# Kernel optimization log

Measured on AMD Instinct MI355X. Metric: run time of the kernel, lower is better.

Reference implementation:

```python
import jax, jax.numpy as jnp
import numpy as np

NUM_HEADS = 16
HEAD_DIM = 64
MAX_REL = 128
NEG_INF = -1e30


def setup_inputs() -> dict:
    key = jax.random.key(0)
    ks = jax.random.split(key, 5)
    B, L, D = 2, 2048, 1024
    x = jax.random.normal(ks[0], (B, L, D), dtype=jnp.float32)
    key_padding_mask = jnp.zeros((B, L), dtype=bool)  # True = padded
    Wqkv = jax.random.normal(ks[1], (D, 3 * D), dtype=jnp.float32) * (D ** -0.5)
    bqkv = jnp.zeros((3 * D,), dtype=jnp.float32)
    Wout = jax.random.normal(ks[2], (D, D), dtype=jnp.float32) * (D ** -0.5)
    bout = jnp.zeros((D,), dtype=jnp.float32)
    bias_table = jax.random.normal(ks[3], (2 * MAX_REL + 1, NUM_HEADS), dtype=jnp.float32) * 0.02
    return {"x": x, "key_padding_mask": key_padding_mask, "Wqkv": Wqkv,
            "bqkv": bqkv, "Wout": Wout, "bout": bout, "bias_table": bias_table}


def _rel_bias(bias_table, L):
    # relative position index: clamp(k - q, -MAX_REL, MAX_REL) + MAX_REL -> [L, L]
    rel = jnp.arange(L)[None, :] - jnp.arange(L)[:, None]
    idx = jnp.clip(rel, -MAX_REL, MAX_REL) + MAX_REL
    return bias_table[idx].transpose(2, 0, 1)  # [H, L, L]


def reference(x, key_padding_mask, Wqkv, bqkv, Wout, bout, bias_table):
    B, L, D = x.shape
    H, hd = NUM_HEADS, HEAD_DIM
    qkv = x @ Wqkv + bqkv                      # [B, L, 3D]
    q, k, v = jnp.split(qkv, 3, axis=-1)
    q = q.reshape(B, L, H, hd).transpose(0, 2, 1, 3)  # [B, H, L, hd]
    k = k.reshape(B, L, H, hd).transpose(0, 2, 1, 3)
    v = v.reshape(B, L, H, hd).transpose(0, 2, 1, 3)
    scores = jnp.einsum('bhqd,bhkd->bhqk', q, k) * (hd ** -0.5)
    scores = scores + _rel_bias(bias_table, L)[None]   # [B, H, L, L]
    scores = jnp.where(key_padding_mask[:, None, None, :], NEG_INF, scores)
    attn = jax.nn.softmax(scores, axis=-1)
    out = jnp.einsum('bhqk,bhkd->bhqd', attn, v)       # [B, H, L, hd]
    out = out.transpose(0, 2, 1, 3).reshape(B, L, D)
    return out @ Wout + bout
```

## Files before the change

### kernel.cpp

```cpp
#include <hip/hip_runtime.h>
#include <hip/hip_bf16.h>
#include <stdint.h>

#define LSEQ 2048
#define BATCH 2
#define DMODEL 1024
#define NH 16
#define HD 64

typedef __attribute__((ext_vector_type(8))) short bf16x8;
typedef __attribute__((ext_vector_type(4))) float f32x4;

__device__ __forceinline__ short f2bf(float f) {
  union { float f; uint32_t u; } v; v.f = f;
  uint32_t r = v.u + 0x8000u;
  return (short)(r >> 16);
}

__device__ __forceinline__ uint32_t pack_bf16(float lo, float hi) {
  union { float f; uint32_t u; } a, b; a.f = lo; b.f = hi;
  uint32_t al = (a.u + 0x8000u) >> 16;
  uint32_t bh = (b.u + 0x8000u) & 0xFFFF0000u;
  return al | bh;
}

__device__ __forceinline__ float exp2_fast(float x) {
#if __has_builtin(__builtin_amdgcn_exp2f)
  return __builtin_amdgcn_exp2f(x);
#else
  float r; asm("v_exp_f32 %0, %1" : "=v"(r) : "v"(x)); return r;
#endif
}

__device__ __forceinline__ void gll16(const void* g, void* l) {
  __builtin_amdgcn_global_load_lds(
      (const __attribute__((address_space(1))) void*)g,
      (__attribute__((address_space(3))) void*)l, 16, 0, 0);
}

__global__ void prep_kernel(const float* __restrict__ x, const float* __restrict__ Wqkv,
                            const float* __restrict__ Wout, short* __restrict__ xbf,
                            short* __restrict__ wqkvT, short* __restrict__ woutT) {
  __shared__ float tile[32][33];
  const int bid = blockIdx.x;
  if (bid < 4096) {
    int i = (bid * 256 + threadIdx.x) * 4;
    float4 v = *(const float4*)(x + i);
    short4 o;
    o.x = f2bf(v.x); o.y = f2bf(v.y); o.z = f2bf(v.z); o.w = f2bf(v.w);
    *(short4*)(xbf + i) = o;
    return;
  }
  const float* in; short* out; int K, N, t;
  if (bid < 7168) { in = Wqkv; out = wqkvT; K = 1024; N = 3072; t = bid - 4096; }
  else            { in = Wout; out = woutT; K = 1024; N = 1024; t = bid - 7168; }
  int kb = (t & 31) * 32, nb = (t >> 5) * 32;
  int tx = threadIdx.x & 31, ty = threadIdx.x >> 5;
  #pragma unroll
  for (int i = ty; i < 32; i += 8)
    tile[i][tx] = in[(size_t)(kb + i) * N + nb + tx];
  __syncthreads();
  #pragma unroll
  for (int i = ty; i < 32; i += 8)
    out[(size_t)(nb + i) * K + kb + tx] = f2bf(tile[tx][i]);
}

template <int EPI>
__global__ __launch_bounds__(256, 2) void gemm_bt(
    const short* __restrict__ A, const short* __restrict__ Bt,
    const float* __restrict__ bias, float* __restrict__ outf,
    short* __restrict__ q_out, short* __restrict__ k_out, short* __restrict__ v_out) {
  constexpr int K = 1024, BK = 64, NKT = K / BK;
  __shared__ short Als[2][128 * BK];
  __shared__ short Bls[2][128 * BK];
  const int tid = threadIdx.x;
  const int lane = tid & 63;
  const int c = lane & 15, g = lane >> 4;
  const int m0 = blockIdx.x * 128;
  const int n0 = blockIdx.y * 128;
  const int wid = tid >> 6;
  const int wm = (wid >> 1) * 64, wn = (wid & 1) * 64;

  f32x4 acc[4][4] = {};

  auto stage = [&](int kt, int bbuf) {
    const int k0 = kt * BK;
    #pragma unroll
    for (int inst = 0; inst < 4; ++inst) {
      int i = inst * 256 + tid;
      int row = i >> 3, cg = i & 7;
      int scc = cg ^ (row & 7);
      gll16(A + (size_t)(m0 + row) * K + k0 + scc * 8, &Als[bbuf][i * 8]);
      gll16(Bt + (size_t)(n0 + row) * K + k0 + scc * 8, &Bls[bbuf][i * 8]);
    }
  };

  stage(0, 0);

  for (int kt = 0; kt < NKT; ++kt) {
    const int bb = kt & 1;
    asm volatile("s_waitcnt vmcnt(0)" ::: "memory");
    __builtin_amdgcn_s_barrier();
    if (kt < NKT - 1) stage(kt + 1, bb ^ 1);

    #pragma unroll
    for (int ks = 0; ks < 2; ++ks) {
      const int kb = ks * 64 + g * 16;
      bf16x8 af[4], bfv[4];
      #pragma unroll
      for (int m = 0; m < 4; ++m) {
        int row = wm + m * 16 + c;
        af[m] = *(const bf16x8*)((const char*)&Als[bb][0] + row * 128 + (kb ^ ((row & 7) << 4)));
      }
      #pragma unroll
      for (int n = 0; n < 4; ++n) {
        int row = wn + n * 16 + c;
        bfv[n] = *(const bf16x8*)((const char*)&Bls[bb][0] + row * 128 + (kb ^ ((row & 7) << 4)));
      }
      __builtin_amdgcn_s_setprio(1);
      #pragma unroll
      for (int m = 0; m < 4; ++m)
        #pragma unroll
        for (int n = 0; n < 4; ++n)
          acc[m][n] = __builtin_amdgcn_mfma_f32_16x16x32_bf16(af[m], bfv[n], acc[m][n], 0, 0, 0);
      __builtin_amdgcn_s_setprio(0);
    }
  }

  #pragma unroll
  for (int m = 0; m < 4; ++m) {
    #pragma unroll
    for (int n = 0; n < 4; ++n) {
      #pragma unroll
      for (int r = 0; r < 4; ++r) {
        int row = m0 + wm + m * 16 + g * 4 + r;
        int col = n0 + wn + n * 16 + c;
        float val = acc[m][n][r] + bias[col];
        if (EPI == 1) {
          outf[(size_t)row * DMODEL + col] = val;
        } else {
          int b = row >> 11, l = row & 2047;
          int which = col >> 10, rem = col & 1023;
          int hn = rem >> 6, d = rem & 63;
          size_t bh = (size_t)b * NH + hn;
          if (which == 0)       q_out[(bh * LSEQ + l) * HD + d] = f2bf(val * 0.1803368801f);
          else if (which == 1)  k_out[(bh * LSEQ + l) * HD + d] = f2bf(val);
          else                  v_out[(bh * HD + d) * LSEQ + l] = f2bf(val);
        }
      }
    }
  }
}

__global__ __launch_bounds__(256, 2) void attn_kernel(
    const short* __restrict__ qb, const short* __restrict__ kb,
    const short* __restrict__ vtb, const unsigned char* __restrict__ kpm,
    const float* __restrict__ bias_table, short* __restrict__ ob) {
  constexpr int NT = LSEQ / 64;
  __shared__ short Kls[2][64 * 64];
  __shared__ short Vls[2][64 * 64];
  __shared__ uint2 Pls[4][512];
  __shared__ float biasc[257];
  __shared__ unsigned mbits_s;

  const int tid = threadIdx.x, lane = tid & 63, wid = tid >> 6;
  const int g = lane >> 4, c = lane & 15;
  const int lin = blockIdx.x;
  const int swz = (lin & 7) * 64 + (lin >> 3);
  const int q0 = (swz & 15) * 128;
  const int h = (swz >> 4) & 15;
  const int b = swz >> 8;
  const size_t bh = (size_t)b * NH + h;
  const short* qbase = qb + bh * LSEQ * HD;
  const short* kbase = kb + bh * LSEQ * HD;
  const short* vbase = vtb + bh * HD * LSEQ;
  const unsigned char* kpmb = kpm + (size_t)b * LSEQ;

  bf16x8 qf[2][2];
  #pragma unroll
  for (int qg = 0; qg < 2; ++qg)
    #pragma unroll
    for (int ks = 0; ks < 2; ++ks) {
      int qrow = q0 + wid * 32 + qg * 16 + c;
      qf[qg][ks] = *(const bf16x8*)(qbase + (size_t)qrow * HD + ks * 32 + g * 8);
    }

  if (tid < 32) {
    const uint4* mp = (const uint4*)(kpmb + tid * 64);
    uint4 m0 = mp[0], m1 = mp[1], m2 = mp[2], m3 = mp[3];
    unsigned anyb = m0.x | m0.y | m0.z | m0.w | m1.x | m1.y | m1.z | m1.w |
                    m2.x | m2.y | m2.z | m2.w | m3.x | m3.y | m3.z | m3.w;
    unsigned long long bal = __ballot(anyb != 0);
    if (tid == 0) mbits_s = (unsigned)bal;
  }
  for (int i = tid; i < 257; i += 256) biasc[i] = bias_table[i * NH + h] * 1.44269504f;
  __syncthreads();
  const unsigned mbits = mbits_s;
  const float cb_lo = biasc[0], cb_hi = biasc[256];

  auto stage = [&](int t, int bbuf) {
    const int kv0s = t * 64;
    #pragma unroll
    for (int inst = 0; inst < 2; ++inst) {
      int cc0 = inst * 256 + tid;
      int row = cc0 >> 3, cc = cc0 & 7;
      int scc = cc ^ (row & 7);
      gll16(kbase + (size_t)(kv0s + row) * HD + scc * 8, &Kls[bbuf][cc0 * 8]);
      gll16(vbase + (size_t)row * LSEQ + kv0s + scc * 8, &Vls[bbuf][cc0 * 8]);
    }
  };

  f32x4 o[4][2], l_acc[2];
  #pragma unroll
  for (int nt = 0; nt < 4; ++nt)
    #pragma unroll
    for (int qg = 0; qg < 2; ++qg) o[nt][qg] = (f32x4){0.f, 0.f, 0.f, 0.f};
  l_acc[0] = (f32x4){0.f, 0.f, 0.f, 0.f};
  l_acc[1] = (f32x4){0.f, 0.f, 0.f, 0.f};

  bf16x8 onesf;
  #pragma unroll
  for (int j = 0; j < 8; ++j) onesf[j] = (short)0x3F80;

  uint2* pw = &Pls[wid][0];
  const int c7s = (c & 7) << 4;
  const int cx  = (c & 7) << 1;

  stage(0, 0);

  for (int t = 0; t < NT; ++t) {
    const int bb = t & 1;
    const int kv0 = t * 64;
    asm volatile("s_waitcnt vmcnt(0)" ::: "memory");
    __builtin_amdgcn_s_barrier();
    if (t < NT - 1) stage(t + 1, bb ^ 1);

    f32x4 st[4][2];
    __builtin_amdgcn_s_setprio(1);
    #pragma unroll
    for (int nt = 0; nt < 4; ++nt) {
      f32x4 a0 = {}, a1 = {};
      #pragma unroll
      for (int ks = 0; ks < 2; ++ks) {
        int krow = nt * 16 + c;
        int kbyte = ks * 64 + g * 16;
        const bf16x8 kf =
            *(const bf16x8*)((const char*)&Kls[bb][0] + krow * 128 + (kbyte ^ c7s));
        a0 = __builtin_amdgcn_mfma_f32_16x16x32_bf16(kf, qf[0][ks], a0, 0, 0, 0);
        a1 = __builtin_amdgcn_mfma_f32_16x16x32_bf16(kf, qf[1][ks], a1, 0, 0, 0);
      }
      st[nt][0] = a0; st[nt][1] = a1;
    }
    __builtin_amdgcn_s_setprio(0);

    const int dw = kv0 - q0 - wid * 32;
    if (dw >= 160 || dw <= -192) {
      const float cb = dw > 0 ? cb_hi : cb_lo;
      #pragma unroll
      for (int nt = 0; nt < 4; ++nt)
        #pragma unroll
        for (int qg = 0; qg < 2; ++qg)
          #pragma unroll
          for (int r = 0; r < 4; ++r) st[nt][qg][r] += cb;
    } else {
      #pragma unroll
      for (int nt = 0; nt < 4; ++nt)
        #pragma unroll
        for (int qg = 0; qg < 2; ++qg) {
          const int base = dw + nt * 16 + g * 4 - qg * 16 - c;
          #pragma unroll
          for (int r = 0; r < 4; ++r) {
            int rel = base + r;
            rel = rel < -128 ? -128 : (rel > 128 ? 128 : rel);
            st[nt][qg][r] += biasc[rel + 128];
          }
        }
    }
    if (mbits & (1u << t)) {
      #pragma unroll
      for (int nt = 0; nt < 4; ++nt)
        #pragma unroll
        for (int r = 0; r < 4; ++r) {
          float mk = kpmb[kv0 + nt * 16 + g * 4 + r] ? -1e30f : 0.f;
          st[nt][0][r] += mk;
          st[nt][1][r] += mk;
        }
    }

    #pragma unroll
    for (int qg = 0; qg < 2; ++qg)
      #pragma unroll
      for (int nt = 0; nt < 4; ++nt) {
        uint2 w;
        w.x = pack_bf16(exp2_fast(st[nt][qg][0]), exp2_fast(st[nt][qg][1]));
        w.y = pack_bf16(exp2_fast(st[nt][qg][2]), exp2_fast(st[nt][qg][3]));
        pw[(qg * 16 + c) * 16 + ((nt * 4 + g) ^ cx)] = w;
      }

    #pragma unroll
    for (int ks = 0; ks < 2; ++ks) {
      const int pu = (ks * 8 + g * 2) ^ cx;
      union { uint2 u[2]; bf16x8 v; } pa0u, pa1u;
      pa0u.u[0] = pw[c * 16 + pu];        pa0u.u[1] = pw[c * 16 + pu + 1];
      pa1u.u[0] = pw[(16 + c) * 16 + pu]; pa1u.u[1] = pw[(16 + c) * 16 + pu + 1];
      const bf16x8 pa0 = pa0u.v, pa1 = pa1u.v;
      l_acc[0] = __builtin_amdgcn_mfma_f32_16x16x32_bf16(pa0, onesf, l_acc[0], 0, 0, 0);
      l_acc[1] = __builtin_amdgcn_mfma_f32_16x16x32_bf16(pa1, onesf, l_acc[1], 0, 0, 0);
      const int pbyte = ks * 64 + g * 16;
      #pragma unroll
      for (int nt = 0; nt < 4; ++nt) {
        int vrow = nt * 16 + c;
        const bf16x8 vf =
            *(const bf16x8*)((const char*)&Vls[bb][0] + vrow * 128 + (pbyte ^ c7s));
        o[nt][0] = __builtin_amdgcn_mfma_f32_16x16x32_bf16(pa0, vf, o[nt][0], 0, 0, 0);
        o[nt][1] = __builtin_amdgcn_mfma_f32_16x16x32_bf16(pa1, vf, o[nt][1], 0, 0, 0);
      }
    }
  }

  #pragma unroll
  for (int qg = 0; qg < 2; ++qg)
    #pragma unroll
    for (int r = 0; r < 4; ++r) {
      float inv = 1.f / l_acc[qg][r];
      int qrow = q0 + wid * 32 + qg * 16 + g * 4 + r;
      size_t obase = ((size_t)b * LSEQ + qrow) * DMODEL + (size_t)h * HD;
      #pragma unroll
      for (int nt = 0; nt < 4; ++nt)
        ob[obase + nt * 16 + c] = f2bf(o[nt][qg][r] * inv);
    }
}

extern "C" void kernel_launch(void* const* d_in, const int* in_sizes, int n_in,
                              void* d_out, int out_size, void* d_ws, size_t ws_size,
                              hipStream_t stream) {
  (void)in_sizes; (void)n_in; (void)out_size; (void)ws_size;
  const float* x = (const float*)d_in[0];
  const unsigned char* kpm = (const unsigned char*)d_in[1];
  const float* Wqkv = (const float*)d_in[2];
  const float* bqkv = (const float*)d_in[3];
  const float* Wout = (const float*)d_in[4];
  const float* bout = (const float*)d_in[5];
  const float* btab = (const float*)d_in[6];
  float* out = (float*)d_out;

  short* ws = (short*)d_ws;
  short* xbf   = ws;
  short* wqkvT = xbf + 4194304;
  short* woutT = wqkvT + 3145728;
  short* qbuf  = woutT + 1048576;
  short* kbuf  = qbuf + 4194304;
  short* vtbuf = kbuf + 4194304;
  short* obuf  = vtbuf + 4194304;

  prep_kernel<<<dim3(8192), dim3(256), 0, stream>>>(x, Wqkv, Wout, xbf, wqkvT, woutT);

  gemm_bt<0><<<dim3(32, 24), dim3(256), 0, stream>>>(xbf, wqkvT, bqkv, nullptr,
                                                     qbuf, kbuf, vtbuf);
  attn_kernel<<<dim3(512), dim3(256), 0, stream>>>(qbuf, kbuf, vtbuf, kpm, btab, obuf);
  gemm_bt<1><<<dim3(32, 8), dim3(256), 0, stream>>>(obuf, woutT, bout, out,
                                                    nullptr, nullptr, nullptr);
}
```

Baseline: 131.6 us.

## Switch attention to 32x32x16 MFMA and pass P through lane shuffles instead of LDS

The attention inner loop now uses 32x32x16 bf16 MFMA tiles instead of 16x16x32. Because the score accumulator layout of the larger tile nearly matches the A-operand layout needed for P·V, the P fragment is rebuilt with cross-half-wave shuffles rather than a write and read round trip through shared memory. This drops the per-wave P buffer and its LDS traffic and issues fewer, larger MFMAs. In exchange it adds shuffle and select work, and the output store pattern changes.

After: 136.1 us. +3.5%, slower.

```diff
diff --git a/kernel.cpp b/kernel.cpp
--- a/kernel.cpp
+++ b/kernel.cpp
@@ -10,6 +10,7 @@
 
 typedef __attribute__((ext_vector_type(8))) short bf16x8;
 typedef __attribute__((ext_vector_type(4))) float f32x4;
+typedef __attribute__((ext_vector_type(16))) float f32x16;
 
 __device__ __forceinline__ short f2bf(float f) {
   union { float f; uint32_t u; } v; v.f = f;
@@ -159,12 +160,12 @@
   constexpr int NT = LSEQ / 64;
   __shared__ short Kls[2][64 * 64];
   __shared__ short Vls[2][64 * 64];
-  __shared__ uint2 Pls[4][512];
   __shared__ float biasc[257];
   __shared__ unsigned mbits_s;
 
   const int tid = threadIdx.x, lane = tid & 63, wid = tid >> 6;
-  const int g = lane >> 4, c = lane & 15;
+  const int l31 = lane & 31, hi = lane >> 5;
+  const bool hib = hi != 0;
   const int lin = blockIdx.x;
   const int swz = (lin & 7) * 64 + (lin >> 3);
   const int q0 = (swz & 15) * 128;
@@ -176,14 +177,11 @@
   const short* vbase = vtb + bh * HD * LSEQ;
   const unsigned char* kpmb = kpm + (size_t)b * LSEQ;
 
-  bf16x8 qf[2][2];
-  #pragma unroll
-  for (int qg = 0; qg < 2; ++qg)
-    #pragma unroll
-    for (int ks = 0; ks < 2; ++ks) {
-      int qrow = q0 + wid * 32 + qg * 16 + c;
-      qf[qg][ks] = *(const bf16x8*)(qbase + (size_t)qrow * HD + ks * 32 + g * 8);
-    }
+  const int qrow_frag = q0 + wid * 32 + l31;
+  bf16x8 qf[4];
+  #pragma unroll
+  for (int ds = 0; ds < 4; ++ds)
+    qf[ds] = *(const bf16x8*)(qbase + (size_t)qrow_frag * HD + ds * 16 + hi * 8);
 
   if (tid < 32) {
     const uint4* mp = (const uint4*)(kpmb + tid * 64);
@@ -210,21 +208,12 @@
     }
   };
 
-  f32x4 o[4][2], l_acc[2];
-  #pragma unroll
-  for (int nt = 0; nt < 4; ++nt)
-    #pragma unroll
-    for (int qg = 0; qg < 2; ++qg) o[nt][qg] = (f32x4){0.f, 0.f, 0.f, 0.f};
-  l_acc[0] = (f32x4){0.f, 0.f, 0.f, 0.f};
-  l_acc[1] = (f32x4){0.f, 0.f, 0.f, 0.f};
+  f32x16 o32[2] = {};
+  f32x16 l32 = {};
 
   bf16x8 onesf;
   #pragma unroll
   for (int j = 0; j < 8; ++j) onesf[j] = (short)0x3F80;
-
-  uint2* pw = &Pls[wid][0];
-  const int c7s = (c & 7) << 4;
-  const int cx  = (c & 7) << 1;
 
   stage(0, 0);
 
@@ -235,100 +224,81 @@
     __builtin_amdgcn_s_barrier();
     if (t < NT - 1) stage(t + 1, bb ^ 1);
 
-    f32x4 st[4][2];
-    __builtin_amdgcn_s_setprio(1);
-    #pragma unroll
-    for (int nt = 0; nt < 4; ++nt) {
-      f32x4 a0 = {}, a1 = {};
-      #pragma unroll
-      for (int ks = 0; ks < 2; ++ks) {
-        int krow = nt * 16 + c;
-        int kbyte = ks * 64 + g * 16;
-        const bf16x8 kf =
-            *(const bf16x8*)((const char*)&Kls[bb][0] + krow * 128 + (kbyte ^ c7s));
-        a0 = __builtin_amdgcn_mfma_f32_16x16x32_bf16(kf, qf[0][ks], a0, 0, 0, 0);
-        a1 = __builtin_amdgcn_mfma_f32_16x16x32_bf16(kf, qf[1][ks], a1, 0, 0, 0);
-      }
-      st[nt][0] = a0; st[nt][1] = a1;
-    }
-    __builtin_amdgcn_s_setprio(0);
-
-    const int dw = kv0 - q0 - wid * 32;
-    if (dw >= 160 || dw <= -192) {
-      const float cb = dw > 0 ? cb_hi : cb_lo;
-      #pragma unroll
-      for (int nt = 0; nt < 4; ++nt)
-        #pragma unroll
-        for (int qg = 0; qg < 2; ++qg)
-          #pragma unroll
-          for (int r = 0; r < 4; ++r) st[nt][qg][r] += cb;
-    } else {
-      #pragma unroll
-      for (int nt = 0; nt < 4; ++nt)
-        #pragma unroll
-        for (int qg = 0; qg < 2; ++qg) {
-          const int base = dw + nt * 16 + g * 4 - qg * 16 - c;
-          #pragma unroll
-          for (int r = 0; r < 4; ++r) {
-            int rel = base + r;
-            rel = rel < -128 ? -128 : (rel > 128 ? 128 : rel);
-            st[nt][qg][r] += biasc[rel + 128];
-          }
+    #pragma unroll
+    for (int kh = 0; kh < 2; ++kh) {
+      f32x16 stv = {};
+      __builtin_amdgcn_s_setprio(1);
+      #pragma unroll
+      for (int ds = 0; ds < 4; ++ds) {
+        const int krow = 32 * kh + l31;
+        const bf16x8 kf = *(const bf16x8*)((const char*)&Kls[bb][0] + krow * 128 +
+                                           ((ds * 32 + hi * 16) ^ ((krow & 7) << 4)));
+        stv = __builtin_amdgcn_mfma_f32_32x32x16_bf16(kf, qf[ds], stv, 0, 0, 0);
+      }
+      __builtin_amdgcn_s_setprio(0);
+
+      const int dq = kv0 + 32 * kh - q0 - wid * 32;
+      float p[16];
+      if (dq >= 159 || dq <= -159) {
+        const float cb = dq > 0 ? cb_hi : cb_lo;
+        #pragma unroll
+        for (int rg = 0; rg < 16; ++rg) p[rg] = stv[rg] + cb;
+      } else {
+        const int base = dq + 4 * hi - l31;
+        #pragma unroll
+        for (int rg = 0; rg < 16; ++rg) {
+          int rel = base + (rg & 3) + 8 * (rg >> 2);
+          rel = rel < -128 ? -128 : (rel > 128 ? 128 : rel);
+          p[rg] = stv[rg] + biasc[rel + 128];
         }
-    }
-    if (mbits & (1u << t)) {
-      #pragma unroll
-      for (int nt = 0; nt < 4; ++nt)
-        #pragma unroll
-        for (int r = 0; r < 4; ++r) {
-          float mk = kpmb[kv0 + nt * 16 + g * 4 + r] ? -1e30f : 0.f;
-          st[nt][0][r] += mk;
-          st[nt][1][r] += mk;
+      }
+      if (mbits & (1u << t)) {
+        #pragma unroll
+        for (int rg = 0; rg < 16; ++rg)
+          p[rg] += kpmb[kv0 + 32 * kh + (rg & 3) + 8 * (rg >> 2) + 4 * hi] ? -1e30f : 0.f;
+      }
+
+      uint32_t W[4][2];
+      #pragma unroll
+      for (int s = 0; s < 4; ++s)
+        #pragma unroll
+        for (int u = 0; u < 2; ++u)
+          W[s][u] = pack_bf16(exp2_fast(p[4 * s + 2 * u]), exp2_fast(p[4 * s + 2 * u + 1]));
+
+      #pragma unroll
+      for (int ktp = 0; ktp < 2; ++ktp) {
+        const int kt = 2 * kh + ktp;
+        const int se = 2 * ktp, so = 2 * ktp + 1;
+        uint32_t recv0 = __shfl_xor(hib ? W[se][0] : W[so][0], 32);
+        uint32_t recv1 = __shfl_xor(hib ? W[se][1] : W[so][1], 32);
+        union { uint32_t u[4]; bf16x8 v; } pa;
+        pa.u[0] = hib ? recv0    : W[se][0];
+        pa.u[1] = hib ? recv1    : W[se][1];
+        pa.u[2] = hib ? W[so][0] : recv0;
+        pa.u[3] = hib ? W[so][1] : recv1;
+
+        __builtin_amdgcn_s_setprio(1);
+        l32 = __builtin_amdgcn_mfma_f32_32x32x16_bf16(pa.v, onesf, l32, 0, 0, 0);
+        #pragma unroll
+        for (int dt = 0; dt < 2; ++dt) {
+          const int vrow = l31 + 32 * dt;
+          const bf16x8 vf = *(const bf16x8*)((const char*)&Vls[bb][0] + vrow * 128 +
+                                             ((kt * 32 + hi * 16) ^ ((vrow & 7) << 4)));
+          o32[dt] = __builtin_amdgcn_mfma_f32_32x32x16_bf16(pa.v, vf, o32[dt], 0, 0, 0);
         }
-    }
-
-    #pragma unroll
-    for (int qg = 0; qg < 2; ++qg)
-      #pragma unroll
-      for (int nt = 0; nt < 4; ++nt) {
-        uint2 w;
-        w.x = pack_bf16(exp2_fast(st[nt][qg][0]), exp2_fast(st[nt][qg][1]));
-        w.y = pack_bf16(exp2_fast(st[nt][qg][2]), exp2_fast(st[nt][qg][3]));
-        pw[(qg * 16 + c) * 16 + ((nt * 4 + g) ^ cx)] = w;
-      }
-
-    #pragma unroll
-    for (int ks = 0; ks < 2; ++ks) {
-      const int pu = (ks * 8 + g * 2) ^ cx;
-      union { uint2 u[2]; bf16x8 v; } pa0u, pa1u;
-      pa0u.u[0] = pw[c * 16 + pu];        pa0u.u[1] = pw[c * 16 + pu + 1];
-      pa1u.u[0] = pw[(16 + c) * 16 + pu]; pa1u.u[1] = pw[(16 + c) * 16 + pu + 1];
-      const bf16x8 pa0 = pa0u.v, pa1 = pa1u.v;
-      l_acc[0] = __builtin_amdgcn_mfma_f32_16x16x32_bf16(pa0, onesf, l_acc[0], 0, 0, 0);
-      l_acc[1] = __builtin_amdgcn_mfma_f32_16x16x32_bf16(pa1, onesf, l_acc[1], 0, 0, 0);
-      const int pbyte = ks * 64 + g * 16;
-      #pragma unroll
-      for (int nt = 0; nt < 4; ++nt) {
-        int vrow = nt * 16 + c;
-        const bf16x8 vf =
-            *(const bf16x8*)((const char*)&Vls[bb][0] + vrow * 128 + (pbyte ^ c7s));
-        o[nt][0] = __builtin_amdgcn_mfma_f32_16x16x32_bf16(pa0, vf, o[nt][0], 0, 0, 0);
-        o[nt][1] = __builtin_amdgcn_mfma_f32_16x16x32_bf16(pa1, vf, o[nt][1], 0, 0, 0);
-      }
-    }
-  }
-
-  #pragma unroll
-  for (int qg = 0; qg < 2; ++qg)
-    #pragma unroll
-    for (int r = 0; r < 4; ++r) {
-      float inv = 1.f / l_acc[qg][r];
-      int qrow = q0 + wid * 32 + qg * 16 + g * 4 + r;
-      size_t obase = ((size_t)b * LSEQ + qrow) * DMODEL + (size_t)h * HD;
-      #pragma unroll
-      for (int nt = 0; nt < 4; ++nt)
-        ob[obase + nt * 16 + c] = f2bf(o[nt][qg][r] * inv);
-    }
+        __builtin_amdgcn_s_setprio(0);
+      }
+    }
+  }
+
+  #pragma unroll
+  for (int rg = 0; rg < 16; ++rg) {
+    const int qrow = q0 + wid * 32 + (rg & 3) + 8 * (rg >> 2) + 4 * hi;
+    const float inv = 1.f / l32[rg];
+    const size_t obase = ((size_t)b * LSEQ + qrow) * DMODEL + (size_t)h * HD + l31;
+    ob[obase]      = f2bf(o32[0][rg] * inv);
+    ob[obase + 32] = f2bf(o32[1][rg] * inv);
+  }
 }
 
 extern "C" void kernel_launch(void* const* d_in, const int* in_sizes, int n_in,
```

## Split attention KV range in two with partial outputs and merge kernel

Applied to the files above, without the earlier changes.

Adds an attention variant that splits each query block's key/value range into two halves. This doubles the block count to 1024, and the kernel runs at a launch bound of 4 blocks per CU with single-buffered K/V LDS. Each half writes unnormalized fp32 partial outputs and row sums, and a separate merge kernel adds them, normalizes, and writes bf16. The aim is more parallelism and occupancy, paid for with extra fp32 global traffic, a second launch, and the loss of the K/V prefetch double buffering. The path is used only when the workspace is large enough; otherwise the original kernel runs.

Result: slower. 149.1 us (+13.4%).

```diff
diff --git a/kernel.cpp b/kernel.cpp
--- a/kernel.cpp
+++ b/kernel.cpp
@@ -152,7 +152,8 @@
   }
 }
 
-__global__ __launch_bounds__(256, 2) void attn_kernel(
+
+__global__ __launch_bounds__(256, 2) void attn_mono(
     const short* __restrict__ qb, const short* __restrict__ kb,
     const short* __restrict__ vtb, const unsigned char* __restrict__ kpm,
     const float* __restrict__ bias_table, short* __restrict__ ob) {
@@ -331,10 +332,212 @@
     }
 }
 
+__global__ __launch_bounds__(256, 4) void attn_split(
+    const short* __restrict__ qb, const short* __restrict__ kb,
+    const short* __restrict__ vtb, const unsigned char* __restrict__ kpm,
+    const float* __restrict__ bias_table, float* __restrict__ part_o,
+    float* __restrict__ part_l) {
+  constexpr int NTL = 16;
+  __shared__ short Kls[64 * 64];
+  __shared__ short Vls[64 * 64];
+  __shared__ uint2 Pls[4][512];
+  __shared__ float biasc[257];
+  __shared__ unsigned mbits_s;
+
+  const int tid = threadIdx.x, lane = tid & 63, wid = tid >> 6;
+  const int g = lane >> 4, c = lane & 15;
+  const int lin = blockIdx.x;
+  const int swz = (lin & 7) * 128 + (lin >> 3);
+  const int q0 = (swz & 15) * 128;
+  const int h = (swz >> 4) & 15;
+  const int b = (swz >> 8) & 1;
+  const int split = swz >> 9;
+  const int kvbase = split * (LSEQ / 2);
+  const size_t bh = (size_t)b * NH + h;
+  const short* qbase = qb + bh * LSEQ * HD;
+  const short* kbase = kb + bh * LSEQ * HD;
+  const short* vbase = vtb + bh * HD * LSEQ;
+  const unsigned char* kpmb = kpm + (size_t)b * LSEQ;
+
+  bf16x8 qf[2][2];
+  #pragma unroll
+  for (int qg = 0; qg < 2; ++qg)
+    #pragma unroll
+    for (int ks = 0; ks < 2; ++ks) {
+      int qrow = q0 + wid * 32 + qg * 16 + c;
+      qf[qg][ks] = *(const bf16x8*)(qbase + (size_t)qrow * HD + ks * 32 + g * 8);
+    }
+
+  if (tid < 32) {
+    const uint4* mp = (const uint4*)(kpmb + tid * 64);
+    uint4 m0 = mp[0], m1 = mp[1], m2 = mp[2], m3 = mp[3];
+    unsigned anyb = m0.x | m0.y | m0.z | m0.w | m1.x | m1.y | m1.z | m1.w |
+                    m2.x | m2.y | m2.z | m2.w | m3.x | m3.y | m3.z | m3.w;
+    unsigned long long bal = __ballot(anyb != 0);
+    if (tid == 0) mbits_s = (unsigned)bal;
+  }
+  for (int i = tid; i < 257; i += 256) biasc[i] = bias_table[i * NH + h] * 1.44269504f;
+  __syncthreads();
+  const unsigned mbits = mbits_s;
+  const float cb_lo = biasc[0], cb_hi = biasc[256];
+
+  auto stage = [&](int t) {
+    const int kv0s = kvbase + t * 64;
+    #pragma unroll
+    for (int inst = 0; inst < 2; ++inst) {
+      int cc0 = inst * 256 + tid;
+      int row = cc0 >> 3, cc = cc0 & 7;
+      int scc = cc ^ (row & 7);
+      gll16(kbase + (size_t)(kv0s + row) * HD + scc * 8, &Kls[cc0 * 8]);
+      gll16(vbase + (size_t)row * LSEQ + kv0s + scc * 8, &Vls[cc0 * 8]);
+    }
+  };
+
+  f32x4 o[4][2], l_acc[2];
+  #pragma unroll
+  for (int nt = 0; nt < 4; ++nt)
+    #pragma unroll
+    for (int qg = 0; qg < 2; ++qg) o[nt][qg] = (f32x4){0.f, 0.f, 0.f, 0.f};
+  l_acc[0] = (f32x4){0.f, 0.f, 0.f, 0.f};
+  l_acc[1] = (f32x4){0.f, 0.f, 0.f, 0.f};
+
+  bf16x8 onesf;
+  #pragma unroll
+  for (int j = 0; j < 8; ++j) onesf[j] = (short)0x3F80;
+
+  uint2* pw = &Pls[wid][0];
+  const int c7s = (c & 7) << 4;
+  const int cx  = (c & 7) << 1;
+
+  for (int t = 0; t < NTL; ++t) {
+    const int kv0 = kvbase + t * 64;
+    __builtin_amdgcn_s_barrier();
+    stage(t);
+    asm volatile("s_waitcnt vmcnt(0)" ::: "memory");
+    __builtin_amdgcn_s_barrier();
+
+    f32x4 st[4][2];
+    __builtin_amdgcn_s_setprio(1);
+    #pragma unroll
+    for (int nt = 0; nt < 4; ++nt) {
+      f32x4 a0 = {}, a1 = {};
+      #pragma unroll
+      for (int ks = 0; ks < 2; ++ks) {
+        int krow = nt * 16 + c;
+        int kbyte = ks * 64 + g * 16;
+        const bf16x8 kf =
+            *(const bf16x8*)((const char*)&Kls[0] + krow * 128 + (kbyte ^ c7s));
+        a0 = __builtin_amdgcn_mfma_f32_16x16x32_bf16(kf, qf[0][ks], a0, 0, 0, 0);
+        a1 = __builtin_amdgcn_mfma_f32_16x16x32_bf16(kf, qf[1][ks], a1, 0, 0, 0);
+      }
+      st[nt][0] = a0; st[nt][1] = a1;
+    }
+    __builtin_amdgcn_s_setprio(0);
+
+    const int dw = kv0 - q0 - wid * 32;
+    if (dw >= 160 || dw <= -192) {
+      const float cb = dw > 0 ? cb_hi : cb_lo;
+      #pragma unroll
+      for (int nt = 0; nt < 4; ++nt)
+        #pragma unroll
+        for (int qg = 0; qg < 2; ++qg)
+          #pragma unroll
+          for (int r = 0; r < 4; ++r) st[nt][qg][r] += cb;
+    } else {
+      #pragma unroll
+      for (int nt = 0; nt < 4; ++nt)
+        #pragma unroll
+        for (int qg = 0; qg < 2; ++qg) {
+          const int base = dw + nt * 16 + g * 4 - qg * 16 - c;
+          #pragma unroll
+          for (int r = 0; r < 4; ++r) {
+            int rel = base + r;
+            rel = rel < -128 ? -128 : (rel > 128 ? 128 : rel);
+            st[nt][qg][r] += biasc[rel + 128];
+          }
+        }
+    }
+    if (mbits & (1u << (kv0 >> 6))) {
+      #pragma unroll
+      for (int nt = 0; nt < 4; ++nt)
+        #pragma unroll
+        for (int r = 0; r < 4; ++r) {
+          float mk = kpmb[kv0 + nt * 16 + g * 4 + r] ? -1e30f : 0.f;
+          st[nt][0][r] += mk;
+          st[nt][1][r] += mk;
+        }
+    }
+
+    #pragma unroll
+    for (int qg = 0; qg < 2; ++qg)
+      #pragma unroll
+      for (int nt = 0; nt < 4; ++nt) {
+        uint2 w;
+        w.x = pack_bf16(exp2_fast(st[nt][qg][0]), exp2_fast(st[nt][qg][1]));
+        w.y = pack_bf16(exp2_fast(st[nt][qg][2]), exp2_fast(st[nt][qg][3]));
+        pw[(qg * 16 + c) * 16 + ((nt * 4 + g) ^ cx)] = w;
+      }
+
+    #pragma unroll
+    for (int ks = 0; ks < 2; ++ks) {
+      const int pu = (ks * 8 + g * 2) ^ cx;
+      union { uint2 u[2]; bf16x8 v; } pa0u, pa1u;
+      pa0u.u[0] = pw[c * 16 + pu];        pa0u.u[1] = pw[c * 16 + pu + 1];
+      pa1u.u[0] = pw[(16 + c) * 16 + pu]; pa1u.u[1] = pw[(16 + c) * 16 + pu + 1];
+      const bf16x8 pa0 = pa0u.v, pa1 = pa1u.v;
+      l_acc[0] = __builtin_amdgcn_mfma_f32_16x16x32_bf16(pa0, onesf, l_acc[0], 0, 0, 0);
+      l_acc[1] = __builtin_amdgcn_mfma_f32_16x16x32_bf16(pa1, onesf, l_acc[1], 0, 0, 0);
+      const int pbyte = ks * 64 + g * 16;
+      #pragma unroll
+      for (int nt = 0; nt < 4; ++nt) {
+        int vrow = nt * 16 + c;
+        const bf16x8 vf =
+            *(const bf16x8*)((const char*)&Vls[0] + vrow * 128 + (pbyte ^ c7s));
+        o[nt][0] = __builtin_amdgcn_mfma_f32_16x16x32_bf16(pa0, vf, o[nt][0], 0, 0, 0);
+        o[nt][1] = __builtin_amdgcn_mfma_f32_16x16x32_bf16(pa1, vf, o[nt][1], 0, 0, 0);
+      }
+    }
+  }
+
+  float* po = part_o + (size_t)split * (BATCH * NH * LSEQ) * HD;
+  float* pl = part_l + (size_t)split * (BATCH * NH * LSEQ);
+  #pragma unroll
+  for (int qg = 0; qg < 2; ++qg)
+    #pragma unroll
+    for (int r = 0; r < 4; ++r) {
+      int qrow = q0 + wid * 32 + qg * 16 + g * 4 + r;
+      size_t row = bh * LSEQ + qrow;
+      #pragma unroll
+      for (int nt = 0; nt < 4; ++nt)
+        po[row * HD + nt * 16 + c] = o[nt][qg][r];
+      if (c == 0) pl[row] = l_acc[qg][r];
+    }
+}
+
+__global__ void merge_kernel(const float* __restrict__ part_o,
+                             const float* __restrict__ part_l,
+                             short* __restrict__ ob) {
+  constexpr size_t HALF = (size_t)BATCH * NH * LSEQ * HD;
+  constexpr size_t ROWS = (size_t)BATCH * NH * LSEQ;
+  size_t i = ((size_t)blockIdx.x * 256 + threadIdx.x) * 4;
+  size_t row = i >> 6;
+  float4 a = *(const float4*)(part_o + i);
+  float4 bvec = *(const float4*)(part_o + HALF + i);
+  float inv = 1.f / (part_l[row] + part_l[ROWS + row]);
+  int bi = (int)(row >> 15), h = (int)((row >> 11) & 15), q = (int)(row & 2047);
+  size_t oidx = (((size_t)bi * LSEQ + q) * DMODEL) + (size_t)h * HD + (i & 63);
+  short4 o;
+  o.x = f2bf((a.x + bvec.x) * inv);
+  o.y = f2bf((a.y + bvec.y) * inv);
+  o.z = f2bf((a.z + bvec.z) * inv);
+  o.w = f2bf((a.w + bvec.w) * inv);
+  *(short4*)(ob + oidx) = o;
+}
+
 extern "C" void kernel_launch(void* const* d_in, const int* in_sizes, int n_in,
                               void* d_out, int out_size, void* d_ws, size_t ws_size,
                               hipStream_t stream) {
-  (void)in_sizes; (void)n_in; (void)out_size; (void)ws_size;
+  (void)in_sizes; (void)n_in; (void)out_size;
   const float* x = (const float*)d_in[0];
   const unsigned char* kpm = (const unsigned char*)d_in[1];
   const float* Wqkv = (const float*)d_in[2];
@@ -352,12 +555,21 @@
   short* kbuf  = qbuf + 4194304;
   short* vtbuf = kbuf + 4194304;
   short* obuf  = vtbuf + 4194304;
+  float* part_o = (float*)(obuf + 4194304);
+  float* part_l = part_o + 2 * (size_t)4194304;
+  const size_t need = (size_t)(obuf + 4194304 - ws) * 2 + 8388608ull * 4 + 131072ull * 4 * 2;
 
   prep_kernel<<<dim3(8192), dim3(256), 0, stream>>>(x, Wqkv, Wout, xbf, wqkvT, woutT);
 
   gemm_bt<0><<<dim3(32, 24), dim3(256), 0, stream>>>(xbf, wqkvT, bqkv, nullptr,
                                                      qbuf, kbuf, vtbuf);
-  attn_kernel<<<dim3(512), dim3(256), 0, stream>>>(qbuf, kbuf, vtbuf, kpm, btab, obuf);
+  if (ws_size >= need) {
+    attn_split<<<dim3(1024), dim3(256), 0, stream>>>(qbuf, kbuf, vtbuf, kpm, btab,
+                                                     part_o, part_l);
+    merge_kernel<<<dim3(4096), dim3(256), 0, stream>>>(part_o, part_l, obuf);
+  } else {
+    attn_mono<<<dim3(512), dim3(256), 0, stream>>>(qbuf, kbuf, vtbuf, kpm, btab, obuf);
+  }
   gemm_bt<1><<<dim3(32, 8), dim3(256), 0, stream>>>(obuf, woutT, bout, out,
                                                     nullptr, nullptr, nullptr);
 }
```

## Load K/V fragments directly from global memory instead of LDS staging

Applied to the files above, without the earlier changes.

Removes the double-buffered LDS staging of K and V tiles, along with the per-tile barrier and wait. Each wave now reads its MFMA operand fragments straight from global memory into registers, and the PV MFMA block is raised to high priority. The aim is to drop LDS traffic and block-wide synchronisation. The cost is that each wave refetches K/V that was previously shared across 4 waves, and load latency is no longer hidden by prefetching.

Measured after the change: 192.4 us. +46.3%, slower.

```diff
diff --git a/kernel.cpp b/kernel.cpp
--- a/kernel.cpp
+++ b/kernel.cpp
@@ -157,8 +157,6 @@
     const short* __restrict__ vtb, const unsigned char* __restrict__ kpm,
     const float* __restrict__ bias_table, short* __restrict__ ob) {
   constexpr int NT = LSEQ / 64;
-  __shared__ short Kls[2][64 * 64];
-  __shared__ short Vls[2][64 * 64];
   __shared__ uint2 Pls[4][512];
   __shared__ float biasc[257];
   __shared__ unsigned mbits_s;
@@ -198,18 +196,6 @@
   const unsigned mbits = mbits_s;
   const float cb_lo = biasc[0], cb_hi = biasc[256];
 
-  auto stage = [&](int t, int bbuf) {
-    const int kv0s = t * 64;
-    #pragma unroll
-    for (int inst = 0; inst < 2; ++inst) {
-      int cc0 = inst * 256 + tid;
-      int row = cc0 >> 3, cc = cc0 & 7;
-      int scc = cc ^ (row & 7);
-      gll16(kbase + (size_t)(kv0s + row) * HD + scc * 8, &Kls[bbuf][cc0 * 8]);
-      gll16(vbase + (size_t)row * LSEQ + kv0s + scc * 8, &Vls[bbuf][cc0 * 8]);
-    }
-  };
-
   f32x4 o[4][2], l_acc[2];
   #pragma unroll
   for (int nt = 0; nt < 4; ++nt)
@@ -223,17 +209,18 @@
   for (int j = 0; j < 8; ++j) onesf[j] = (short)0x3F80;
 
   uint2* pw = &Pls[wid][0];
-  const int c7s = (c & 7) << 4;
-  const int cx  = (c & 7) << 1;
-
-  stage(0, 0);
+  const int cx = (c & 7) << 1;
 
   for (int t = 0; t < NT; ++t) {
-    const int bb = t & 1;
     const int kv0 = t * 64;
-    asm volatile("s_waitcnt vmcnt(0)" ::: "memory");
-    __builtin_amdgcn_s_barrier();
-    if (t < NT - 1) stage(t + 1, bb ^ 1);
+
+    bf16x8 kfr[4][2];
+    #pragma unroll
+    for (int nt = 0; nt < 4; ++nt)
+      #pragma unroll
+      for (int ks = 0; ks < 2; ++ks)
+        kfr[nt][ks] = *(const bf16x8*)(kbase + (size_t)(kv0 + nt * 16 + c) * HD +
+                                       ks * 32 + g * 8);
 
     f32x4 st[4][2];
     __builtin_amdgcn_s_setprio(1);
@@ -242,12 +229,8 @@
       f32x4 a0 = {}, a1 = {};
       #pragma unroll
       for (int ks = 0; ks < 2; ++ks) {
-        int krow = nt * 16 + c;
-        int kbyte = ks * 64 + g * 16;
-        const bf16x8 kf =
-            *(const bf16x8*)((const char*)&Kls[bb][0] + krow * 128 + (kbyte ^ c7s));
-        a0 = __builtin_amdgcn_mfma_f32_16x16x32_bf16(kf, qf[0][ks], a0, 0, 0, 0);
-        a1 = __builtin_amdgcn_mfma_f32_16x16x32_bf16(kf, qf[1][ks], a1, 0, 0, 0);
+        a0 = __builtin_amdgcn_mfma_f32_16x16x32_bf16(kfr[nt][ks], qf[0][ks], a0, 0, 0, 0);
+        a1 = __builtin_amdgcn_mfma_f32_16x16x32_bf16(kfr[nt][ks], qf[1][ks], a1, 0, 0, 0);
       }
       st[nt][0] = a0; st[nt][1] = a1;
     }
@@ -299,22 +282,25 @@
 
     #pragma unroll
     for (int ks = 0; ks < 2; ++ks) {
+      bf16x8 vfr[4];
+      #pragma unroll
+      for (int nt = 0; nt < 4; ++nt)
+        vfr[nt] = *(const bf16x8*)(vbase + (size_t)(nt * 16 + c) * LSEQ + kv0 +
+                                   ks * 32 + g * 8);
       const int pu = (ks * 8 + g * 2) ^ cx;
       union { uint2 u[2]; bf16x8 v; } pa0u, pa1u;
       pa0u.u[0] = pw[c * 16 + pu];        pa0u.u[1] = pw[c * 16 + pu + 1];
       pa1u.u[0] = pw[(16 + c) * 16 + pu]; pa1u.u[1] = pw[(16 + c) * 16 + pu + 1];
       const bf16x8 pa0 = pa0u.v, pa1 = pa1u.v;
+      __builtin_amdgcn_s_setprio(1);
       l_acc[0] = __builtin_amdgcn_mfma_f32_16x16x32_bf16(pa0, onesf, l_acc[0], 0, 0, 0);
       l_acc[1] = __builtin_amdgcn_mfma_f32_16x16x32_bf16(pa1, onesf, l_acc[1], 0, 0, 0);
-      const int pbyte = ks * 64 + g * 16;
       #pragma unroll
       for (int nt = 0; nt < 4; ++nt) {
-        int vrow = nt * 16 + c;
-        const bf16x8 vf =
-            *(const bf16x8*)((const char*)&Vls[bb][0] + vrow * 128 + (pbyte ^ c7s));
-        o[nt][0] = __builtin_amdgcn_mfma_f32_16x16x32_bf16(pa0, vf, o[nt][0], 0, 0, 0);
-        o[nt][1] = __builtin_amdgcn_mfma_f32_16x16x32_bf16(pa1, vf, o[nt][1], 0, 0, 0);
-      }
+        o[nt][0] = __builtin_amdgcn_mfma_f32_16x16x32_bf16(pa0, vfr[nt], o[nt][0], 0, 0, 0);
+        o[nt][1] = __builtin_amdgcn_mfma_f32_16x16x32_bf16(pa1, vfr[nt], o[nt][1], 0, 0, 0);
+      }
+      __builtin_amdgcn_s_setprio(0);
     }
   }
 
```
